# Optimization experiments

Measured on AMD Instinct MI355X. Metric: run time of the kernel, lower is better.

The kernel has to match this reference:

```python
import jax, jax.numpy as jnp
import numpy as np

STEP_SIZE = 0.01
ITERATION = 1.0
F_FORCING = 8.0
N_STEPS = int(round(ITERATION / STEP_SIZE))  # 100 fixed RK4 steps

BATCH = 8192
INPUT_SIZE = 784
SYSTEM_COUNT = 1024
OUTPUT_SIZE = 10


def setup_inputs() -> dict:
    key = jax.random.key(0)
    k_x, k_w1, k_b1, k_w2, k_b2 = jax.random.split(key, 5)
    x = jax.random.normal(k_x, (BATCH, INPUT_SIZE), dtype=jnp.float32)
    # nn.Linear-style params (out_features, in_features)
    s1 = 1.0 / np.sqrt(INPUT_SIZE)
    W1 = jax.random.uniform(k_w1, (SYSTEM_COUNT, INPUT_SIZE), jnp.float32, -s1, s1)
    b1 = jax.random.uniform(k_b1, (SYSTEM_COUNT,), jnp.float32, -s1, s1)
    s2 = 1.0 / np.sqrt(SYSTEM_COUNT)
    W2 = jax.random.uniform(k_w2, (OUTPUT_SIZE, SYSTEM_COUNT), jnp.float32, -s2, s2)
    b2 = jax.random.uniform(k_b2, (OUTPUT_SIZE,), jnp.float32, -s2, s2)
    return {"x": x, "W1": W1, "b1": b1, "W2": W2, "b2": b2}


def _lorenz96(x):
    # (roll(x,-1) - roll(x,2)) * roll(x,1) - x + F   along feature dim 1
    return (jnp.roll(x, -1, axis=1) - jnp.roll(x, 2, axis=1)) * jnp.roll(x, 1, axis=1) - x + F_FORCING


def _rk4_integrate(x0):
    h = jnp.float32(STEP_SIZE)

    def step(x, _):
        k1 = _lorenz96(x)
        k2 = _lorenz96(x + 0.5 * h * k1)
        k3 = _lorenz96(x + 0.5 * h * k2)
        k4 = _lorenz96(x + h * k3)
        x_next = x + (h / 6.0) * (k1 + 2.0 * k2 + 2.0 * k3 + k4)
        return x_next, None

    xT, _ = jax.lax.scan(step, x0, None, length=N_STEPS)
    return xT


def reference(x, W1, b1, W2, b2):
    h = x @ W1.T + b1                 # [B, systemCount]
    h = _rk4_integrate(h)             # RK4 over [0, iteration], step 0.01
    logits = h @ W2.T + b2            # [B, output_size]
    return jax.nn.log_softmax(logits, axis=1)
```

## Files before the change

kernel.cpp:

```cpp
#include <hip/hip_runtime.h>
#include <hip/hip_bf16.h>
#include <math.h>

#define BATCH 8192
#define INSZ 784
#define SYS 1024
#define OUTSZ 10
#define NSTEP 100
#define HSTEP 0.01f
#define FFORCE 8.0f
#define KP 800

typedef short short8 __attribute__((ext_vector_type(8)));
typedef float float4v __attribute__((ext_vector_type(4)));
typedef float v2f __attribute__((ext_vector_type(2)));

static __device__ __forceinline__ short f2bf(float x) {
    __hip_bfloat16 b = __float2bfloat16(x);
    return __builtin_bit_cast(short, b);
}
static __device__ __forceinline__ float bf2f(short s) {
    unsigned int u = ((unsigned int)(unsigned short)s) << 16;
    return __builtin_bit_cast(float, u);
}

static __device__ __forceinline__ v2f pkfma(v2f a, v2f b, v2f c) {
    return __builtin_elementwise_fma(a, b, c);
}
static __device__ __forceinline__ v2f mk2(float x, float y) {
    v2f r; r.x = x; r.y = y; return r;
}
static __device__ __forceinline__ v2f sh2(v2f v, int ln) {
    v2f r; r.x = __shfl(v.x, ln); r.y = __shfl(v.y, ln); return r;
}

__global__ __launch_bounds__(256) void convert_kernel(
    const float* __restrict__ x, const float* __restrict__ W1,
    short* __restrict__ xh, short* __restrict__ xl,
    short* __restrict__ wh, short* __restrict__ wl)
{
    const int total = (BATCH + SYS) * (KP / 8);
    for (int idx = blockIdx.x * blockDim.x + threadIdx.x; idx < total;
         idx += gridDim.x * blockDim.x) {
        const int row = idx / (KP / 8);
        const int ck  = idx - row * (KP / 8);

        short8 hi, lo;
        if (ck < INSZ / 8) {
            const float* src = (row < BATCH)
                ? (x + (size_t)row * INSZ)
                : (W1 + (size_t)(row - BATCH) * INSZ);
            float4 v0 = ((const float4*)src)[ck * 2];
            float4 v1 = ((const float4*)src)[ck * 2 + 1];
            float vv[8] = {v0.x, v0.y, v0.z, v0.w, v1.x, v1.y, v1.z, v1.w};
            #pragma unroll
            for (int j = 0; j < 8; ++j) {
                short hj = f2bf(vv[j]);
                hi[j] = hj;
                lo[j] = f2bf(vv[j] - bf2f(hj));
            }
        } else {
            #pragma unroll
            for (int j = 0; j < 8; ++j) { hi[j] = 0; lo[j] = 0; }
        }

        short* dh; short* dl;
        if (row < BATCH) {
            dh = xh + (size_t)row * KP;
            dl = xl + (size_t)row * KP;
        } else {
            dh = wh + (size_t)(row - BATCH) * KP;
            dl = wl + (size_t)(row - BATCH) * KP;
        }
        *(short8*)(dh + ck * 8) = hi;
        *(short8*)(dl + ck * 8) = lo;
    }
}

#define BM3 128
#define BN3 128
#define BK3 32
#define LDK3 40

__global__ __launch_bounds__(512, 2) void gemm1s_kernel(
    const short* __restrict__ xh, const short* __restrict__ xl,
    const short* __restrict__ wh, const short* __restrict__ wl,
    const float* __restrict__ b1, float* __restrict__ h)
{
    __shared__ short Ah[BM3 * LDK3], Al[BM3 * LDK3];
    __shared__ short Bh[BN3 * LDK3], Bl[BN3 * LDK3];

    const int t  = threadIdx.x;
    const int bm = blockIdx.y * BM3;
    const int bn = blockIdx.x * BN3;

    const int srow = t >> 2;
    const int kq   = (t & 3) * 8;

    const int wv   = t >> 6;
    const int wr   = wv >> 1;
    const int wc   = wv & 1;
    const int lane = t & 63;
    const int lm   = lane & 15;
    const int q    = lane >> 4;

    float4v acc[2][4];
    #pragma unroll
    for (int mi = 0; mi < 2; ++mi)
        #pragma unroll
        for (int nj = 0; nj < 4; ++nj) {
            acc[mi][nj][0] = 0.f; acc[mi][nj][1] = 0.f;
            acc[mi][nj][2] = 0.f; acc[mi][nj][3] = 0.f;
        }

    const short* pxh = xh + (size_t)(bm + srow) * KP + kq;
    const short* pxl = xl + (size_t)(bm + srow) * KP + kq;
    const short* pwh = wh + (size_t)(bn + srow) * KP + kq;
    const short* pwl = wl + (size_t)(bn + srow) * KP + kq;
    const int sbase = srow * LDK3 + kq;

    short8 ra = *(const short8*)(pxh);
    short8 rb = *(const short8*)(pxl);
    short8 rc = *(const short8*)(pwh);
    short8 rd = *(const short8*)(pwl);

    for (int it = 0; it < 25; ++it) {
        *(short8*)&Ah[sbase] = ra;
        *(short8*)&Al[sbase] = rb;
        *(short8*)&Bh[sbase] = rc;
        *(short8*)&Bl[sbase] = rd;
        __syncthreads();

        if (it < 24) {
            const int k1 = (it + 1) * BK3;
            ra = *(const short8*)(pxh + k1);
            rb = *(const short8*)(pxl + k1);
            rc = *(const short8*)(pwh + k1);
            rd = *(const short8*)(pwl + k1);
        }

        short8 fah[2], fal[2];
        #pragma unroll
        for (int mi = 0; mi < 2; ++mi) {
            const int ao = (wr * 32 + mi * 16 + lm) * LDK3 + q * 8;
            fah[mi] = *(const short8*)&Ah[ao];
            fal[mi] = *(const short8*)&Al[ao];
        }
        #pragma unroll
        for (int nj = 0; nj < 4; ++nj) {
            const int bo = (wc * 64 + nj * 16 + lm) * LDK3 + q * 8;
            short8 bh = *(const short8*)&Bh[bo];
            short8 bl = *(const short8*)&Bl[bo];
            #pragma unroll
            for (int mi = 0; mi < 2; ++mi) {
                acc[mi][nj] = __builtin_amdgcn_mfma_f32_16x16x32_bf16(fah[mi], bh, acc[mi][nj], 0, 0, 0);
                acc[mi][nj] = __builtin_amdgcn_mfma_f32_16x16x32_bf16(fah[mi], bl, acc[mi][nj], 0, 0, 0);
                acc[mi][nj] = __builtin_amdgcn_mfma_f32_16x16x32_bf16(fal[mi], bh, acc[mi][nj], 0, 0, 0);
            }
        }
        __syncthreads();
    }

    #pragma unroll
    for (int mi = 0; mi < 2; ++mi) {
        const int row0 = bm + wr * 32 + mi * 16 + q * 4;
        #pragma unroll
        for (int nj = 0; nj < 4; ++nj) {
            const int col  = bn + wc * 64 + nj * 16 + lm;
            const float bias = b1[col];
            #pragma unroll
            for (int r = 0; r < 4; ++r)
                h[(size_t)(row0 + r) * SYS + col] = acc[mi][nj][r] + bias;
        }
    }
}

#define BM2 64
#define BN2 64
#define BK2 32
#define LDK2 40

__global__ __launch_bounds__(256, 4) void gemm1_kernel(
    const float* __restrict__ x, const float* __restrict__ W1,
    const float* __restrict__ b1, float* __restrict__ h)
{
    __shared__ short Ah[BM2 * LDK2], Al[BM2 * LDK2];
    __shared__ short Bh[BN2 * LDK2], Bl[BN2 * LDK2];

    const int t  = threadIdx.x;
    const int bm = blockIdx.y * BM2;
    const int bn = blockIdx.x * BN2;

    const int srow = t >> 2;
    const int kq   = (t & 3) * 8;

    const int wv   = t >> 6;
    const int lane = t & 63;
    const int lm   = lane & 15;
    const int q    = lane >> 4;

    float4v acc[4];
    #pragma unroll
    for (int j = 0; j < 4; ++j) {
        acc[j][0] = 0.f; acc[j][1] = 0.f; acc[j][2] = 0.f; acc[j][3] = 0.f;
    }

    const float* xa0 = x  + (size_t)(bm + srow) * INSZ + kq;
    const float* wb0 = W1 + (size_t)(bn + srow) * INSZ + kq;

    for (int it = 0; it < 25; ++it) {
        const int k0 = it * BK2;
        {
            const bool valid = (k0 + kq) < INSZ;
            float va[8], vb[8];
            if (valid) {
                #pragma unroll
                for (int p = 0; p < 2; ++p) {
                    float4 xv = ((const float4*)(xa0 + k0))[p];
                    float4 bv = ((const float4*)(wb0 + k0))[p];
                    va[4*p+0] = xv.x; va[4*p+1] = xv.y; va[4*p+2] = xv.z; va[4*p+3] = xv.w;
                    vb[4*p+0] = bv.x; vb[4*p+1] = bv.y; vb[4*p+2] = bv.z; vb[4*p+3] = bv.w;
                }
            } else {
                #pragma unroll
                for (int j = 0; j < 8; ++j) { va[j] = 0.f; vb[j] = 0.f; }
            }
            short8 ahi, alo, bhi, blo;
            #pragma unroll
            for (int j = 0; j < 8; ++j) {
                short h1 = f2bf(va[j]);
                short l1 = f2bf(va[j] - bf2f(h1));
                short h2 = f2bf(vb[j]);
                short l2 = f2bf(vb[j] - bf2f(h2));
                ahi[j] = h1;  alo[j] = l1;
                bhi[j] = h2;  blo[j] = l2;
            }
            const int base = srow * LDK2 + kq;
            *(short8*)&Ah[base] = ahi;
            *(short8*)&Al[base] = alo;
            *(short8*)&Bh[base] = bhi;
            *(short8*)&Bl[base] = blo;
        }
        __syncthreads();

        const int aoff = (wv * 16 + lm) * LDK2 + q * 8;
        short8 ah = *(const short8*)&Ah[aoff];
        short8 al = *(const short8*)&Al[aoff];
        #pragma unroll
        for (int fj = 0; fj < 4; ++fj) {
            const int boff = (fj * 16 + lm) * LDK2 + q * 8;
            short8 bh = *(const short8*)&Bh[boff];
            short8 bl = *(const short8*)&Bl[boff];
            acc[fj] = __builtin_amdgcn_mfma_f32_16x16x32_bf16(ah, bh, acc[fj], 0, 0, 0);
            acc[fj] = __builtin_amdgcn_mfma_f32_16x16x32_bf16(ah, bl, acc[fj], 0, 0, 0);
            acc[fj] = __builtin_amdgcn_mfma_f32_16x16x32_bf16(al, bh, acc[fj], 0, 0, 0);
        }
        __syncthreads();
    }

    #pragma unroll
    for (int fj = 0; fj < 4; ++fj) {
        const int col  = bn + fj * 16 + lm;
        const float bias = b1[col];
        const int row0 = bm + wv * 16 + q * 4;
        #pragma unroll
        for (int r = 0; r < 4; ++r)
            h[(size_t)(row0 + r) * SYS + col] = acc[fj][r] + bias;
    }
}

__global__ __launch_bounds__(256, 4) void rk4_kernel(
    const float* __restrict__ hbuf, const float* __restrict__ W2,
    const float* __restrict__ b2, float* __restrict__ out)
{
    const int lane = threadIdx.x & 63;
    const int w    = threadIdx.x >> 6;
    const int rowA = blockIdx.x * 8 + w * 2;
    const int rowB = rowA + 1;

    const int laneL = (lane + 63) & 63;
    const int laneR = (lane + 1) & 63;

    v2f X[16];
    {
        const float4* a4 = (const float4*)(hbuf + (size_t)rowA * SYS) + lane * 4;
        const float4* b4 = (const float4*)(hbuf + (size_t)rowB * SYS) + lane * 4;
        #pragma unroll
        for (int k = 0; k < 4; ++k) {
            float4 av = a4[k], bv = b4[k];
            X[4*k+0] = mk2(av.x, bv.x);
            X[4*k+1] = mk2(av.y, bv.y);
            X[4*k+2] = mk2(av.z, bv.z);
            X[4*k+3] = mk2(av.w, bv.w);
        }
    }

    const v2f Fv     = mk2(FFORCE, FFORCE);
    const v2f c_half = mk2(0.5f * HSTEP, 0.5f * HSTEP);
    const v2f c_full = mk2(HSTEP, HSTEP);
    const v2f c_two  = mk2(2.0f, 2.0f);
    const v2f c_six  = mk2(HSTEP / 6.0f, HSTEP / 6.0f);

    v2f acc[16], T[16];

    auto deriv_ip = [&](v2f (&y)[16], v2f r1, v2f l1, v2f l2) {
        v2f y0o = y[0], y1o = y[1], y2o = y[2];
        v2f d0 = Fv - y[0], d1 = Fv - y[1], d15 = Fv - y[15];
        v2f p2 = y0o, p1 = y1o, cur = y[2];
        #pragma unroll
        for (int i = 2; i < 15; ++i) {
            v2f yp1 = (i < 14) ? y[i + 1] : y[15];
            v2f nv  = pkfma(yp1 - p2, p1, Fv - cur);
            p2 = p1; p1 = cur;
            if (i < 14) cur = y[i + 1];
            y[i] = nv;
        }
        y[15] = pkfma(r1 - p2, p1, d15);
        y[1]  = pkfma(y2o - l1, y0o, d1);
        y[0]  = pkfma(y1o - l2, l1, d0);
    };

    v2f r1x = sh2(X[0],  laneR);
    v2f l1x = sh2(X[15], laneL);
    v2f l2x = sh2(X[14], laneL);

    #pragma unroll 1
    for (int s = 0; s < NSTEP; ++s) {
        #pragma unroll
        for (int i = 2; i < 15; ++i)
            acc[i] = pkfma(X[i + 1] - X[i - 2], X[i - 1], Fv - X[i]);
        acc[15] = pkfma(r1x - X[13], X[14], Fv - X[15]);
        acc[1]  = pkfma(X[2] - l1x, X[0],  Fv - X[1]);
        acc[0]  = pkfma(X[1] - l2x, l1x,   Fv - X[0]);

        T[14] = pkfma(c_half, acc[14], X[14]);
        T[15] = pkfma(c_half, acc[15], X[15]);
        T[0]  = pkfma(c_half, acc[0],  X[0]);
        v2f r1 = sh2(T[0],  laneR);
        v2f l1 = sh2(T[15], laneL);
        v2f l2 = sh2(T[14], laneL);
        #pragma unroll
        for (int i = 1; i < 14; ++i) T[i] = pkfma(c_half, acc[i], X[i]);
        deriv_ip(T, r1, l1, l2);

        {
            v2f a;
            a = T[14]; acc[14] = pkfma(c_two, a, acc[14]); T[14] = pkfma(c_half, a, X[14]);
            a = T[15]; acc[15] = pkfma(c_two, a, acc[15]); T[15] = pkfma(c_half, a, X[15]);
            a = T[0];  acc[0]  = pkfma(c_two, a, acc[0]);  T[0]  = pkfma(c_half, a, X[0]);
            r1 = sh2(T[0],  laneR);
            l1 = sh2(T[15], laneL);
            l2 = sh2(T[14], laneL);
            #pragma unroll
            for (int i = 1; i < 14; ++i) {
                a = T[i]; acc[i] = pkfma(c_two, a, acc[i]); T[i] = pkfma(c_half, a, X[i]);
            }
        }
        deriv_ip(T, r1, l1, l2);

        {
            v2f a;
            a = T[14]; acc[14] = pkfma(c_two, a, acc[14]); T[14] = pkfma(c_full, a, X[14]);
            a = T[15]; acc[15] = pkfma(c_two, a, acc[15]); T[15] = pkfma(c_full, a, X[15]);
            a = T[0];  acc[0]  = pkfma(c_two, a, acc[0]);  T[0]  = pkfma(c_full, a, X[0]);
            r1 = sh2(T[0],  laneR);
            l1 = sh2(T[15], laneL);
            l2 = sh2(T[14], laneL);
            #pragma unroll
            for (int i = 1; i < 14; ++i) {
                a = T[i]; acc[i] = pkfma(c_two, a, acc[i]); T[i] = pkfma(c_full, a, X[i]);
            }
        }
        deriv_ip(T, r1, l1, l2);

        X[14] = pkfma(c_six, acc[14] + T[14], X[14]);
        X[15] = pkfma(c_six, acc[15] + T[15], X[15]);
        X[0]  = pkfma(c_six, acc[0]  + T[0],  X[0]);
        r1x = sh2(X[0],  laneR);
        l1x = sh2(X[15], laneL);
        l2x = sh2(X[14], laneL);
        #pragma unroll
        for (int i = 1; i < 14; ++i)
            X[i] = pkfma(c_six, acc[i] + T[i], X[i]);
    }

    v2f l[OUTSZ];
    #pragma unroll
    for (int o = 0; o < OUTSZ; ++o) {
        const float4* w4 = (const float4*)(W2 + (size_t)o * SYS) + lane * 4;
        v2f s2 = mk2(0.f, 0.f);
        #pragma unroll
        for (int k = 0; k < 4; ++k) {
            float4 wv = w4[k];
            s2 = pkfma(X[4*k+0], mk2(wv.x, wv.x), s2);
            s2 = pkfma(X[4*k+1], mk2(wv.y, wv.y), s2);
            s2 = pkfma(X[4*k+2], mk2(wv.z, wv.z), s2);
            s2 = pkfma(X[4*k+3], mk2(wv.w, wv.w), s2);
        }
        #pragma unroll
        for (int dlt = 1; dlt < 64; dlt <<= 1) {
            s2.x += __shfl_xor(s2.x, dlt);
            s2.y += __shfl_xor(s2.y, dlt);
        }
        const float bo = b2[o];
        l[o] = s2 + mk2(bo, bo);
    }

    v2f m = l[0];
    #pragma unroll
    for (int o = 1; o < OUTSZ; ++o) m = __builtin_elementwise_max(m, l[o]);
    v2f ssum = mk2(0.f, 0.f);
    #pragma unroll
    for (int o = 0; o < OUTSZ; ++o) {
        v2f d = l[o] - m;
        ssum = ssum + mk2(__expf(d.x), __expf(d.y));
    }
    const v2f lse = m + mk2(__logf(ssum.x), __logf(ssum.y));

    float vA = l[0].x - lse.x;
    float vB = l[0].y - lse.y;
    #pragma unroll
    for (int o = 1; o < OUTSZ; ++o) {
        if (lane == o) { vA = l[o].x - lse.x; vB = l[o].y - lse.y; }
    }
    if (lane < OUTSZ) {
        out[(size_t)rowA * OUTSZ + lane] = vA;
        out[(size_t)rowB * OUTSZ + lane] = vB;
    }
}

extern "C" void kernel_launch(void* const* d_in, const int* in_sizes, int n_in,
                              void* d_out, int out_size, void* d_ws, size_t ws_size,
                              hipStream_t stream)
{
    const float* x  = (const float*)d_in[0];
    const float* W1 = (const float*)d_in[1];
    const float* b1 = (const float*)d_in[2];
    const float* W2 = (const float*)d_in[3];
    const float* b2 = (const float*)d_in[4];
    float* out = (float*)d_out;
    float* h   = (float*)d_ws;

    const size_t hbytes      = (size_t)BATCH * SYS * sizeof(float);
    const size_t splitshorts = (size_t)(BATCH + SYS) * KP;
    const size_t need        = hbytes + 2 * splitshorts * sizeof(short);

    if (ws_size >= need) {
        short* xh = (short*)((char*)d_ws + hbytes);
        short* xl = xh + (size_t)BATCH * KP;
        short* wh = xl + (size_t)BATCH * KP;
        short* wl = wh + (size_t)SYS * KP;
        convert_kernel<<<2048, 256, 0, stream>>>(x, W1, xh, xl, wh, wl);
        dim3 g1(SYS / BN3, BATCH / BM3);
        gemm1s_kernel<<<g1, 512, 0, stream>>>(xh, xl, wh, wl, b1, h);
    } else {
        dim3 g1(SYS / BN2, BATCH / BM2);
        gemm1_kernel<<<g1, 256, 0, stream>>>(x, W1, b1, h);
    }

    rk4_kernel<<<BATCH / 8, 256, 0, stream>>>(h, W2, b2, out);
}
```

Baseline: 425.7 us.

## Use direct global-to-LDS loads and swizzled block order in GEMM1

The first GEMM now loads tiles straight from global memory into LDS with global_load_lds, replacing the register staging and explicit LDS stores. All fragments are read into registers before the next tile load is issued, so the tile load overlaps the MFMA work. Block indices are swizzled for L2 locality, and the launch bound asks for 4 blocks per CU. The LDS padding is removed, which may add bank conflicts on fragment reads. GEMM1 is only part of a run dominated by the RK4 integration, so the end-to-end effect is limited.

```diff
diff --git a/kernel.cpp b/kernel.cpp
--- a/kernel.cpp
+++ b/kernel.cpp
@@ -32,6 +32,12 @@
 }
 static __device__ __forceinline__ v2f sh2(v2f v, int ln) {
     v2f r; r.x = __shfl(v.x, ln); r.y = __shfl(v.y, ln); return r;
+}
+
+static __device__ __forceinline__ void gld_lds16(const void* g, void* l) {
+    __builtin_amdgcn_global_load_lds(
+        (const __attribute__((address_space(1))) unsigned int*)g,
+        (__attribute__((address_space(3))) unsigned int*)l, 16, 0, 0);
 }
 
 __global__ __launch_bounds__(256) void convert_kernel(
@@ -80,27 +86,30 @@
 #define BM3 128
 #define BN3 128
 #define BK3 32
-#define LDK3 40
-
-__global__ __launch_bounds__(512, 2) void gemm1s_kernel(
+
+__global__ __launch_bounds__(512, 4) void gemm1s_kernel(
     const short* __restrict__ xh, const short* __restrict__ xl,
     const short* __restrict__ wh, const short* __restrict__ wl,
     const float* __restrict__ b1, float* __restrict__ h)
 {
-    __shared__ short Ah[BM3 * LDK3], Al[BM3 * LDK3];
-    __shared__ short Bh[BN3 * LDK3], Bl[BN3 * LDK3];
-
-    const int t  = threadIdx.x;
-    const int bm = blockIdx.y * BM3;
-    const int bn = blockIdx.x * BN3;
+    __shared__ short Ah[BM3 * BK3], Al[BM3 * BK3];
+    __shared__ short Bh[BN3 * BK3], Bl[BN3 * BK3];
+
+    const int t = threadIdx.x;
+
+    const int lin = blockIdx.y * gridDim.x + blockIdx.x;
+    const int nwg = gridDim.x * gridDim.y;
+    const int cpx = nwg >> 3;
+    const int swz = (lin & 7) * cpx + (lin >> 3);
+    const int bm  = (swz >> 3) * BM3;
+    const int bn  = (swz & 7) * BN3;
 
     const int srow = t >> 2;
-    const int kq   = (t & 3) * 8;
-
     const int wv   = t >> 6;
+    const int lane = t & 63;
+
     const int wr   = wv >> 1;
     const int wc   = wv & 1;
-    const int lane = t & 63;
     const int lm   = lane & 15;
     const int q    = lane >> 4;
 
@@ -113,52 +122,56 @@
             acc[mi][nj][2] = 0.f; acc[mi][nj][3] = 0.f;
         }
 
-    const short* pxh = xh + (size_t)(bm + srow) * KP + kq;
-    const short* pxl = xl + (size_t)(bm + srow) * KP + kq;
-    const short* pwh = wh + (size_t)(bn + srow) * KP + kq;
-    const short* pwl = wl + (size_t)(bn + srow) * KP + kq;
-    const int sbase = srow * LDK3 + kq;
-
-    short8 ra = *(const short8*)(pxh);
-    short8 rb = *(const short8*)(pxl);
-    short8 rc = *(const short8*)(pwh);
-    short8 rd = *(const short8*)(pwl);
+    const short* gxh = xh + (size_t)(bm + srow) * KP + (t & 3) * 8;
+    const short* gxl = xl + (size_t)(bm + srow) * KP + (t & 3) * 8;
+    const short* gwh = wh + (size_t)(bn + srow) * KP + (t & 3) * 8;
+    const short* gwl = wl + (size_t)(bn + srow) * KP + (t & 3) * 8;
+
+    short* lAh = &Ah[wv * 512];
+    short* lAl = &Al[wv * 512];
+    short* lBh = &Bh[wv * 512];
+    short* lBl = &Bl[wv * 512];
+
+    gld_lds16(gxh, lAh);
+    gld_lds16(gxl, lAl);
+    gld_lds16(gwh, lBh);
+    gld_lds16(gwl, lBl);
 
     for (int it = 0; it < 25; ++it) {
-        *(short8*)&Ah[sbase] = ra;
-        *(short8*)&Al[sbase] = rb;
-        *(short8*)&Bh[sbase] = rc;
-        *(short8*)&Bl[sbase] = rd;
+        __syncthreads();
+
+        short8 fah[2], fal[2], fbh[4], fbl[4];
+        #pragma unroll
+        for (int mi = 0; mi < 2; ++mi) {
+            const int ao = (wr * 32 + mi * 16 + lm) * BK3 + q * 8;
+            fah[mi] = *(const short8*)&Ah[ao];
+            fal[mi] = *(const short8*)&Al[ao];
+        }
+        #pragma unroll
+        for (int nj = 0; nj < 4; ++nj) {
+            const int bo = (wc * 64 + nj * 16 + lm) * BK3 + q * 8;
+            fbh[nj] = *(const short8*)&Bh[bo];
+            fbl[nj] = *(const short8*)&Bl[bo];
+        }
         __syncthreads();
 
         if (it < 24) {
             const int k1 = (it + 1) * BK3;
-            ra = *(const short8*)(pxh + k1);
-            rb = *(const short8*)(pxl + k1);
-            rc = *(const short8*)(pwh + k1);
-            rd = *(const short8*)(pwl + k1);
-        }
-
-        short8 fah[2], fal[2];
-        #pragma unroll
-        for (int mi = 0; mi < 2; ++mi) {
-            const int ao = (wr * 32 + mi * 16 + lm) * LDK3 + q * 8;
-            fah[mi] = *(const short8*)&Ah[ao];
-            fal[mi] = *(const short8*)&Al[ao];
-        }
+            gld_lds16(gxh + k1, lAh);
+            gld_lds16(gxl + k1, lAl);
+            gld_lds16(gwh + k1, lBh);
+            gld_lds16(gwl + k1, lBl);
+        }
+
         #pragma unroll
         for (int nj = 0; nj < 4; ++nj) {
-            const int bo = (wc * 64 + nj * 16 + lm) * LDK3 + q * 8;
-            short8 bh = *(const short8*)&Bh[bo];
-            short8 bl = *(const short8*)&Bl[bo];
             #pragma unroll
             for (int mi = 0; mi < 2; ++mi) {
-                acc[mi][nj] = __builtin_amdgcn_mfma_f32_16x16x32_bf16(fah[mi], bh, acc[mi][nj], 0, 0, 0);
-                acc[mi][nj] = __builtin_amdgcn_mfma_f32_16x16x32_bf16(fah[mi], bl, acc[mi][nj], 0, 0, 0);
-                acc[mi][nj] = __builtin_amdgcn_mfma_f32_16x16x32_bf16(fal[mi], bh, acc[mi][nj], 0, 0, 0);
-            }
-        }
-        __syncthreads();
+                acc[mi][nj] = __builtin_amdgcn_mfma_f32_16x16x32_bf16(fah[mi], fbh[nj], acc[mi][nj], 0, 0, 0);
+                acc[mi][nj] = __builtin_amdgcn_mfma_f32_16x16x32_bf16(fah[mi], fbl[nj], acc[mi][nj], 0, 0, 0);
+                acc[mi][nj] = __builtin_amdgcn_mfma_f32_16x16x32_bf16(fal[mi], fbh[nj], acc[mi][nj], 0, 0, 0);
+            }
+        }
     }
 
     #pragma unroll
```

After: 419.5 us. About the same (-1.4%).
